# Kernel optimization log

Hardware: AMD Instinct MI355X
Metric: run time of the kernel (lower is better)

The kernel has to match this reference:

```python
import jax, jax.numpy as jnp
import numpy as np


def setup_inputs() -> dict:
    key = jax.random.key(0)
    k1, k2 = jax.random.split(key)
    B, D, K = 4096, 64, 50000
    x = jax.random.normal(k1, (B, D), dtype=jnp.float32)
    weight = jax.random.normal(k2, (D, K), dtype=jnp.float32)
    return {"x": x, "weight": weight}


def reference(x, weight):
    # output[b, j] = || x[b, :] - weight[:, j] ||_2
    # avoiding the [B, D, K] intermediate the original materializes.
    x2 = jnp.sum(x * x, axis=1, keepdims=True)            # [B, 1]
    w2 = jnp.sum(weight * weight, axis=0, keepdims=True)  # [1, K]
    xw = x @ weight                                       # [B, K]
    sq = jnp.maximum(x2 + w2 - 2.0 * xw, 1e-12)
    return jnp.sqrt(sq)                                   # [B, K]
```

## Files before the change

kernel.cpp:

```cpp
#include <hip/hip_runtime.h>
#include <hip/hip_bf16.h>


typedef __bf16 bf16x8 __attribute__((ext_vector_type(8)));
typedef float floatx4 __attribute__((ext_vector_type(4)));
typedef float float4v __attribute__((ext_vector_type(4)));
typedef unsigned short ushortx4 __attribute__((ext_vector_type(4)));
typedef unsigned short ushortx8 __attribute__((ext_vector_type(8)));
typedef short short8 __attribute__((ext_vector_type(8)));

constexpr int Bb = 4096;
constexpr int Dd = 64;
constexpr int Kk = 50000;
constexpr int BM = 128;
constexpr int BN = 128;
constexpr int LDA = 72;

__device__ __forceinline__ unsigned short f2bf(float f) {
  union { float f; unsigned u; } v; v.f = f;
  unsigned r = v.u + 0x7FFFu + ((v.u >> 16) & 1u);
  return (unsigned short)(r >> 16);
}
__device__ __forceinline__ float bf2f(unsigned short h) {
  union { unsigned u; float f; } v; v.u = ((unsigned)h) << 16;
  return v.f;
}

__global__ void euclid_kernel(const float* __restrict__ x,
                              const float* __restrict__ w,
                              float* __restrict__ out) {
  __shared__ alignas(16) unsigned short As[BM * LDA];
  __shared__ alignas(16) unsigned short Bs[BN * LDA];
  __shared__ float x2s[BM];
  __shared__ float w2s[BN];

  const int tid = threadIdx.x;
  const int m0 = blockIdx.x * BM;
  const int j0 = blockIdx.y * BN;

  {
    const float4v* x4 = (const float4v*)(x + (size_t)m0 * Dd);
#pragma unroll
    for (int it = 0; it < (BM * Dd / 4) / 256; ++it) {
      int i = it * 256 + tid;
      float4v v = x4[i];
      int r = i >> 4;
      int q = i & 15;
      ushortx4 h;
      h.x = f2bf(v.x); h.y = f2bf(v.y); h.z = f2bf(v.z); h.w = f2bf(v.w);
      *(ushortx4*)&As[r * LDA + q * 4] = h;
    }
  }

  {
    int c = tid & 127;
    int gc = j0 + c;
    bool valid = gc < Kk;
    const float* wp = w + gc;
#pragma unroll
    for (int k = (tid >> 7) * 2; k < Dd; k += 4) {
      float v0 = valid ? wp[(size_t)k * Kk] : 0.0f;
      float v1 = valid ? wp[(size_t)(k + 1) * Kk] : 0.0f;
      unsigned pack = (unsigned)f2bf(v0) | ((unsigned)f2bf(v1) << 16);
      *(unsigned*)&Bs[c * LDA + k] = pack;
    }
  }
  __syncthreads();

  if (tid < BM) {
    float s = 0.f;
#pragma unroll
    for (int kq = 0; kq < 8; ++kq) {
      ushortx8 u = *(const ushortx8*)&As[tid * LDA + kq * 8];
#pragma unroll
      for (int j = 0; j < 8; ++j) { float v = bf2f(u[j]); s = fmaf(v, v, s); }
    }
    x2s[tid] = s;
  } else {
    int c = tid - BM;
    float s = 0.f;
#pragma unroll
    for (int kq = 0; kq < 8; ++kq) {
      ushortx8 u = *(const ushortx8*)&Bs[c * LDA + kq * 8];
#pragma unroll
      for (int j = 0; j < 8; ++j) { float v = bf2f(u[j]); s = fmaf(v, v, s); }
    }
    w2s[c] = s;
  }
  __syncthreads();

  const int wv = tid >> 6;
  const int lane = tid & 63;
  const int l15 = lane & 15;
  const int quad = lane >> 4;

  bf16x8 a[2][2];
#pragma unroll
  for (int mi = 0; mi < 2; ++mi)
#pragma unroll
    for (int kc = 0; kc < 2; ++kc)
      a[mi][kc] = *(const bf16x8*)&As[(32 * wv + 16 * mi + l15) * LDA + kc * 32 + quad * 8];

  floatx4 acc[2][8];
#pragma unroll
  for (int mi = 0; mi < 2; ++mi)
#pragma unroll
    for (int ni = 0; ni < 8; ++ni)
      acc[mi][ni] = (floatx4){0.f, 0.f, 0.f, 0.f};

#pragma unroll
  for (int ni = 0; ni < 8; ++ni) {
    bf16x8 b0 = *(const bf16x8*)&Bs[(16 * ni + l15) * LDA + quad * 8];
    bf16x8 b1 = *(const bf16x8*)&Bs[(16 * ni + l15) * LDA + 32 + quad * 8];
#pragma unroll
    for (int mi = 0; mi < 2; ++mi) {
      acc[mi][ni] = __builtin_amdgcn_mfma_f32_16x16x32_bf16(a[mi][0], b0, acc[mi][ni], 0, 0, 0);
      acc[mi][ni] = __builtin_amdgcn_mfma_f32_16x16x32_bf16(a[mi][1], b1, acc[mi][ni], 0, 0, 0);
    }
  }

  float xn[2][4];
#pragma unroll
  for (int mi = 0; mi < 2; ++mi)
#pragma unroll
    for (int r = 0; r < 4; ++r)
      xn[mi][r] = x2s[32 * wv + 16 * mi + quad * 4 + r];

#pragma unroll
  for (int ni = 0; ni < 8; ++ni) {
    int col = 16 * ni + l15;
    int gcol = j0 + col;
    if (gcol >= Kk) continue;
    float w2 = w2s[col];
#pragma unroll
    for (int mi = 0; mi < 2; ++mi) {
      int rbase = 32 * wv + 16 * mi + quad * 4;
#pragma unroll
      for (int r = 0; r < 4; ++r) {
        float sq = xn[mi][r] + w2 - 2.0f * acc[mi][ni][r];
        sq = fmaxf(sq, 1e-12f);
        out[(size_t)(m0 + rbase + r) * Kk + gcol] = sqrtf(sq);
      }
    }
  }
}

extern "C" void kernel_launch(void* const* d_in, const int* in_sizes, int n_in,
                              void* d_out, int out_size, void* d_ws, size_t ws_size,
                              hipStream_t stream) {
  const float* x = (const float*)d_in[0];
  const float* w = (const float*)d_in[1];
  float* out = (float*)d_out;
  dim3 grid(Bb / BM, (Kk + BN - 1) / BN);
  euclid_kernel<<<grid, dim3(256), 0, stream>>>(x, w, out);
}
```

Before: 1.062 ms.

## Load x directly into MFMA registers and emit vectorized nontemporal float4 stores

Removes the shared-memory staging of x: each lane loads its bf16 A fragments straight from global memory and computes the row norms with wave shuffles. The w norms are now computed during the load pass, which drops a barrier and the separate norm pass. The MFMA operands are swapped so each lane holds 4 consecutive output columns, allowing 16-byte nontemporal stores instead of scalar strided stores. It also adds launch bounds and uses the fast sqrt builtin. This relies on K being a multiple of 4 for the float4 store guard and alignment.

```diff
diff --git a/kernel.cpp b/kernel.cpp
--- a/kernel.cpp
+++ b/kernel.cpp
@@ -1,13 +1,9 @@
 #include <hip/hip_runtime.h>
-#include <hip/hip_bf16.h>
 
 
 typedef __bf16 bf16x8 __attribute__((ext_vector_type(8)));
 typedef float floatx4 __attribute__((ext_vector_type(4)));
 typedef float float4v __attribute__((ext_vector_type(4)));
-typedef unsigned short ushortx4 __attribute__((ext_vector_type(4)));
-typedef unsigned short ushortx8 __attribute__((ext_vector_type(8)));
-typedef short short8 __attribute__((ext_vector_type(8)));
 
 constexpr int Bb = 4096;
 constexpr int Dd = 64;
@@ -26,68 +22,15 @@
   return v.f;
 }
 
-__global__ void euclid_kernel(const float* __restrict__ x,
-                              const float* __restrict__ w,
-                              float* __restrict__ out) {
-  __shared__ alignas(16) unsigned short As[BM * LDA];
+__global__ __launch_bounds__(256, 4) void euclid_kernel(
+    const float* __restrict__ x, const float* __restrict__ w,
+    float* __restrict__ out) {
   __shared__ alignas(16) unsigned short Bs[BN * LDA];
-  __shared__ float x2s[BM];
-  __shared__ float w2s[BN];
+  __shared__ alignas(16) float w2p[2][BN];
 
   const int tid = threadIdx.x;
   const int m0 = blockIdx.x * BM;
   const int j0 = blockIdx.y * BN;
-
-  {
-    const float4v* x4 = (const float4v*)(x + (size_t)m0 * Dd);
-#pragma unroll
-    for (int it = 0; it < (BM * Dd / 4) / 256; ++it) {
-      int i = it * 256 + tid;
-      float4v v = x4[i];
-      int r = i >> 4;
-      int q = i & 15;
-      ushortx4 h;
-      h.x = f2bf(v.x); h.y = f2bf(v.y); h.z = f2bf(v.z); h.w = f2bf(v.w);
-      *(ushortx4*)&As[r * LDA + q * 4] = h;
-    }
-  }
-
-  {
-    int c = tid & 127;
-    int gc = j0 + c;
-    bool valid = gc < Kk;
-    const float* wp = w + gc;
-#pragma unroll
-    for (int k = (tid >> 7) * 2; k < Dd; k += 4) {
-      float v0 = valid ? wp[(size_t)k * Kk] : 0.0f;
-      float v1 = valid ? wp[(size_t)(k + 1) * Kk] : 0.0f;
-      unsigned pack = (unsigned)f2bf(v0) | ((unsigned)f2bf(v1) << 16);
-      *(unsigned*)&Bs[c * LDA + k] = pack;
-    }
-  }
-  __syncthreads();
-
-  if (tid < BM) {
-    float s = 0.f;
-#pragma unroll
-    for (int kq = 0; kq < 8; ++kq) {
-      ushortx8 u = *(const ushortx8*)&As[tid * LDA + kq * 8];
-#pragma unroll
-      for (int j = 0; j < 8; ++j) { float v = bf2f(u[j]); s = fmaf(v, v, s); }
-    }
-    x2s[tid] = s;
-  } else {
-    int c = tid - BM;
-    float s = 0.f;
-#pragma unroll
-    for (int kq = 0; kq < 8; ++kq) {
-      ushortx8 u = *(const ushortx8*)&Bs[c * LDA + kq * 8];
-#pragma unroll
-      for (int j = 0; j < 8; ++j) { float v = bf2f(u[j]); s = fmaf(v, v, s); }
-    }
-    w2s[c] = s;
-  }
-  __syncthreads();
 
   const int wv = tid >> 6;
   const int lane = tid & 63;
@@ -95,52 +38,92 @@
   const int quad = lane >> 4;
 
   bf16x8 a[2][2];
+  float x2r[2];
 #pragma unroll
-  for (int mi = 0; mi < 2; ++mi)
+  for (int ri = 0; ri < 2; ++ri) {
+    const int grow = m0 + 32 * wv + 16 * ri + l15;
+    const float4v* xp = (const float4v*)(x + (size_t)grow * Dd);
+    float s = 0.f;
 #pragma unroll
-    for (int kc = 0; kc < 2; ++kc)
-      a[mi][kc] = *(const bf16x8*)&As[(32 * wv + 16 * mi + l15) * LDA + kc * 32 + quad * 8];
+    for (int kc = 0; kc < 2; ++kc) {
+      float4v v0 = xp[kc * 8 + quad * 2];
+      float4v v1 = xp[kc * 8 + quad * 2 + 1];
+      union { bf16x8 v; unsigned short us[8]; } u;
+      u.us[0] = f2bf(v0.x); u.us[1] = f2bf(v0.y);
+      u.us[2] = f2bf(v0.z); u.us[3] = f2bf(v0.w);
+      u.us[4] = f2bf(v1.x); u.us[5] = f2bf(v1.y);
+      u.us[6] = f2bf(v1.z); u.us[7] = f2bf(v1.w);
+#pragma unroll
+      for (int j = 0; j < 8; ++j) {
+        float rv = bf2f(u.us[j]);
+        s = fmaf(rv, rv, s);
+      }
+      a[ri][kc] = u.v;
+    }
+    s += __shfl_xor(s, 16);
+    s += __shfl_xor(s, 32);
+    x2r[ri] = s;
+  }
+
+  {
+    const int c = tid & 127;
+    const int g = tid >> 7;
+    const int gc = j0 + c;
+    const bool valid = gc < Kk;
+    const float* wp = w + gc;
+    float s = 0.f;
+#pragma unroll
+    for (int k = 2 * g; k < Dd; k += 4) {
+      float v0 = valid ? wp[(size_t)k * Kk] : 0.0f;
+      float v1 = valid ? wp[(size_t)(k + 1) * Kk] : 0.0f;
+      unsigned short h0 = f2bf(v0), h1 = f2bf(v1);
+      float r0 = bf2f(h0), r1 = bf2f(h1);
+      s = fmaf(r0, r0, s);
+      s = fmaf(r1, r1, s);
+      *(unsigned*)&Bs[c * LDA + k] = (unsigned)h0 | ((unsigned)h1 << 16);
+    }
+    w2p[g][c] = s;
+  }
+  __syncthreads();
 
   floatx4 acc[2][8];
 #pragma unroll
-  for (int mi = 0; mi < 2; ++mi)
+  for (int ri = 0; ri < 2; ++ri)
 #pragma unroll
-    for (int ni = 0; ni < 8; ++ni)
-      acc[mi][ni] = (floatx4){0.f, 0.f, 0.f, 0.f};
+    for (int ci = 0; ci < 8; ++ci)
+      acc[ri][ci] = (floatx4){0.f, 0.f, 0.f, 0.f};
 
 #pragma unroll
-  for (int ni = 0; ni < 8; ++ni) {
-    bf16x8 b0 = *(const bf16x8*)&Bs[(16 * ni + l15) * LDA + quad * 8];
-    bf16x8 b1 = *(const bf16x8*)&Bs[(16 * ni + l15) * LDA + 32 + quad * 8];
+  for (int ci = 0; ci < 8; ++ci) {
+    bf16x8 b0 = *(const bf16x8*)&Bs[(16 * ci + l15) * LDA + quad * 8];
+    bf16x8 b1 = *(const bf16x8*)&Bs[(16 * ci + l15) * LDA + 32 + quad * 8];
 #pragma unroll
-    for (int mi = 0; mi < 2; ++mi) {
-      acc[mi][ni] = __builtin_amdgcn_mfma_f32_16x16x32_bf16(a[mi][0], b0, acc[mi][ni], 0, 0, 0);
-      acc[mi][ni] = __builtin_amdgcn_mfma_f32_16x16x32_bf16(a[mi][1], b1, acc[mi][ni], 0, 0, 0);
+    for (int ri = 0; ri < 2; ++ri) {
+      acc[ri][ci] = __builtin_amdgcn_mfma_f32_16x16x32_bf16(b0, a[ri][0], acc[ri][ci], 0, 0, 0);
+      acc[ri][ci] = __builtin_amdgcn_mfma_f32_16x16x32_bf16(b1, a[ri][1], acc[ri][ci], 0, 0, 0);
     }
   }
 
-  float xn[2][4];
 #pragma unroll
-  for (int mi = 0; mi < 2; ++mi)
+  for (int ri = 0; ri < 2; ++ri) {
+    const int grow = m0 + 32 * wv + 16 * ri + l15;
+    float* po = out + (size_t)grow * Kk + j0 + quad * 4;
+    const float xx = x2r[ri];
 #pragma unroll
-    for (int r = 0; r < 4; ++r)
-      xn[mi][r] = x2s[32 * wv + 16 * mi + quad * 4 + r];
-
-#pragma unroll
-  for (int ni = 0; ni < 8; ++ni) {
-    int col = 16 * ni + l15;
-    int gcol = j0 + col;
-    if (gcol >= Kk) continue;
-    float w2 = w2s[col];
-#pragma unroll
-    for (int mi = 0; mi < 2; ++mi) {
-      int rbase = 32 * wv + 16 * mi + quad * 4;
+    for (int ci = 0; ci < 8; ++ci) {
+      const int gcol = j0 + 16 * ci + quad * 4;
+      if (gcol >= Kk) continue;
+      float4v wq0 = *(const float4v*)&w2p[0][16 * ci + quad * 4];
+      float4v wq1 = *(const float4v*)&w2p[1][16 * ci + quad * 4];
+      float4v o;
 #pragma unroll
       for (int r = 0; r < 4; ++r) {
-        float sq = xn[mi][r] + w2 - 2.0f * acc[mi][ni][r];
+        float t = xx + (wq0[r] + wq1[r]);
+        float sq = fmaf(-2.0f, acc[ri][ci][r], t);
         sq = fmaxf(sq, 1e-12f);
-        out[(size_t)(m0 + rbase + r) * Kk + gcol] = sqrtf(sq);
+        o[r] = __builtin_amdgcn_sqrtf(sq);
       }
+      __builtin_nontemporal_store(o, (float4v*)(po + 16 * ci));
     }
   }
 }
```

New measurement: 991.8 us. 1.07x faster.
